# Optimization experiments

Hardware: AMD Instinct MI355X
Metric: run time of the kernel (lower is better)

## Reference

```python
import jax, jax.numpy as jnp
import numpy as np

N_NODES = 50000
N_EDGES = 800000
IN_CH = 256
OUT_CH = 128
HID = 2 * OUT_CH  # 256
LN_EPS = 1e-5


def _add_self_loops(edge_index, n):
    loop = jnp.arange(n, dtype=edge_index.dtype)
    src = jnp.concatenate([edge_index[0], loop])
    dst = jnp.concatenate([edge_index[1], loop])
    return src, dst


def _gcn_norm(src, dst, n):
    # PyG GCNConv norm: deg over source index, symmetric normalization
    ones = jnp.ones(src.shape[0], dtype=jnp.float32)
    deg = jax.ops.segment_sum(ones, src, num_segments=n)
    dinv = jnp.where(deg > 0, deg ** -0.5, 0.0)
    return dinv[src] * dinv[dst]  # [E+N]


def _gcn_conv(x, src, dst, norm, w, b, gamma=None, beta=None):
    h = x @ w                              # [N, out]
    msgs = norm[:, None] * h[src]          # gather + scale, [E+N, out]
    out = jax.ops.segment_sum(msgs, dst, num_segments=x.shape[0])
    if gamma is not None:
        out = gamma * out + beta           # FiLM modulation (per-feature)
    return out + b


def _layernorm(x):
    mu = jnp.mean(x, axis=-1, keepdims=True)
    var = jnp.var(x, axis=-1, keepdims=True)
    return (x - mu) * jax.lax.rsqrt(var + LN_EPS)


def setup_inputs() -> dict:
    key = jax.random.key(0)
    ks = jax.random.split(key, 20)

    def g(k, shape, scale=0.05):
        return jax.random.normal(k, shape, dtype=jnp.float32) * scale

    x = jax.random.normal(ks[0], (N_NODES, IN_CH), dtype=jnp.float32)
    edge_index = jax.random.randint(ks[1], (2, N_EDGES), 0, N_NODES, dtype=jnp.int64)
    return {
        "x": x,
        "edge_index": edge_index,
        "conv1_w": g(ks[2], (IN_CH, HID)),
        "conv1_b": g(ks[3], (HID,)),
        "conv2_w": g(ks[4], (HID, OUT_CH)),
        "conv2_b": g(ks[5], (OUT_CH,)),
        "sig_conv_w": g(ks[6], (IN_CH, HID)),
        "sig_conv_b": g(ks[7], (HID,)),
        "fc1_w": g(ks[8], (HID, HID)),
        "fc1_b": g(ks[9], (HID,)),
        "fc2_w": g(ks[10], (HID, HID)),
        "fc2_b": g(ks[11], (HID,)),
        "fc3_w": g(ks[12], (OUT_CH, HID)),
        "fc3_b": g(ks[13], (OUT_CH,)),
        "fc4_w": g(ks[14], (OUT_CH, HID)),
        "fc4_b": g(ks[15], (OUT_CH,)),
    }


def reference(x, edge_index, conv1_w, conv1_b, conv2_w, conv2_b,
              sig_conv_w, sig_conv_b, fc1_w, fc1_b, fc2_w, fc2_b,
              fc3_w, fc3_b, fc4_w, fc4_b):
    n = x.shape[0]
    src, dst = _add_self_loops(edge_index, n)
    norm = _gcn_norm(src, dst, n)

    # --- GraphSignature (use_gcn_sig=True) ---
    s = jax.nn.relu(_gcn_conv(x, src, dst, norm, sig_conv_w, sig_conv_b))
    s = s.sum(0)  # [HID]
    gamma1 = jnp.tanh(s @ fc1_w.T + fc1_b)  # [HID]
    beta1 = jnp.tanh(s @ fc2_w.T + fc2_b)   # [HID]
    gamma2 = jnp.tanh(s @ fc3_w.T + fc3_b)  # [OUT]
    beta2 = jnp.tanh(s @ fc4_w.T + fc4_b)   # [OUT]

    # inner_loop=True: signature outputs are detached
    gamma1, beta1, gamma2, beta2 = map(jax.lax.stop_gradient,
                                       (gamma1, beta1, gamma2, beta2))

    # --- Encoder (GAE) ---
    h = jax.nn.relu(_gcn_conv(x, src, dst, norm, conv1_w, conv1_b,
                              gamma=gamma1, beta=beta1))
    h = _layernorm(h)
    out = _gcn_conv(h, src, dst, norm, conv2_w, conv2_b,
                    gamma=gamma2, beta=beta2)
    out = _layernorm(out)
    return out
```

## Files before the change

### kernel.cpp

```cpp
#include <hip/hip_runtime.h>

typedef _Float16 f16;
typedef f16 f16x8 __attribute__((ext_vector_type(8)));
typedef float f32x4 __attribute__((ext_vector_type(4)));
typedef unsigned short u16;
typedef unsigned int u32;

#define IN_CH  256
#define HID    256
#define OUT_CH 128
#define LN_EPS 1e-5f
#define NSLOT  32
#define NR     4
#define NC     64
#define RS     12544
#define HT     512


__global__ __launch_bounds__(HT) void k_hist(const int* __restrict__ ei, int nE, int nN,
                                             int* __restrict__ hP) {
    __shared__ int h[RS];
    int r = blockIdx.x & (NR - 1), c = blockIdx.x >> 2;
    int rsz = (nN + NR - 1) / NR;
    int r0 = r * rsz;
    int sz = nN - r0; if (sz > rsz) sz = rsz;
    for (int i = threadIdx.x; i < sz; i += HT) h[i] = 0;
    __syncthreads();
    int nT = nE + nN;
    int chunk = (nT + NC - 1) / NC;
    int e0 = c * chunk, e1 = e0 + chunk; if (e1 > nT) e1 = nT;
    for (int eb = e0 + (int)threadIdx.x; eb < e1; eb += HT * 4) {
        int ss[4], dd[4];
        #pragma unroll
        for (int u = 0; u < 4; u++) {
            int e = eb + u * HT;
            ss[u] = -1; dd[u] = -1;
            if (e < e1) {
                if (e < nE) { ss[u] = ei[e]; dd[u] = ei[nE + e]; }
                else { ss[u] = e - nE; dd[u] = e - nE; }
            }
        }
        #pragma unroll
        for (int u = 0; u < 4; u++) {
            if ((unsigned)(ss[u] - r0) < (unsigned)sz) atomicAdd(&h[ss[u] - r0], 1);
            if ((unsigned)(dd[u] - r0) < (unsigned)sz) atomicAdd(&h[dd[u] - r0], 0x10000);
        }
    }
    __syncthreads();
    for (int i = threadIdx.x; i < sz; i += HT) hP[(size_t)c * nN + r0 + i] = h[i];
}


__global__ __launch_bounds__(256) void k_alloc(const int* __restrict__ hP,
                                               int* __restrict__ rowstart,
                                               int* __restrict__ chunkbase,
                                               int* __restrict__ cnt_tot,
                                               float* __restrict__ dinv,
                                               int* __restrict__ ctr, int nN,
                                               const float* __restrict__ x, f16* __restrict__ xh,
                                               int nelem, int nAllocB, int nCast,
                                               const float* __restrict__ sigw,
                                               const float* __restrict__ c1w,
                                               const float* __restrict__ c2w,
                                               f16* __restrict__ Wt1, f16* __restrict__ Wt2) {
    int bid = blockIdx.x;
    if (bid < nAllocB) {
        int i = bid * 256 + threadIdx.x;
        int lane = threadIdx.x & 63;
        int cnt = 0, dg = 0;
        if (i < nN) {
            for (int c = 0; c < NC; c++) {
                unsigned pk = (unsigned)hP[(size_t)c * nN + i];
                cnt += (int)(pk >> 16);
                dg  += (int)(pk & 0xffffu);
            }
        }
        int p = cnt;
        #pragma unroll
        for (int off = 1; off < 64; off <<= 1) {
            int v = __shfl_up(p, off, 64);
            if (lane >= off) p += v;
        }
        int tot = __shfl(p, 63, 64);
        int base = 0;
        if (lane == 0) base = atomicAdd(ctr, tot);
        base = __shfl(base, 0, 64);
        if (i < nN) {
            int nb = base + p - cnt;
            rowstart[i] = nb;
            cnt_tot[i] = cnt;
            dinv[i] = rsqrtf((float)dg);
            int run = nb;
            for (int c = 0; c < NC; c++) {
                chunkbase[(size_t)c * nN + i] = run;
                run += (int)((unsigned)hP[(size_t)c * nN + i] >> 16);
            }
        }
    } else if (bid < nAllocB + nCast) {
        int i = (bid - nAllocB) * 2048 + threadIdx.x * 8;
        if (i >= nelem) return;
        float4 a = *(const float4*)(x + i);
        float4 b = *(const float4*)(x + i + 4);
        f16x8 o = { (f16)a.x, (f16)a.y, (f16)a.z, (f16)a.w,
                    (f16)b.x, (f16)b.y, (f16)b.z, (f16)b.w };
        *(f16x8*)(xh + i) = o;
    } else {
        int i = (bid - nAllocB - nCast) * 256 + threadIdx.x;
        if (i < 16384) {
            int ct = i >> 9;
            int rem = i & 511;
            int kx = rem >> 6;
            int lane = rem & 63;
            int q = lane >> 4, l = lane & 15;
            int n = (ct & 15) * 16 + l;
            int k0 = kx * 32 + q * 8;
            const float* src = (ct < 16) ? sigw : c1w;
            f16x8 o;
            #pragma unroll
            for (int j = 0; j < 8; j++) o[j] = (f16)src[(size_t)(k0 + j) * 256 + n];
            *(f16x8*)(Wt1 + (size_t)i * 8) = o;
        } else {
            int h = i - 16384;
            int ct = h >> 9;
            int rem = h & 511;
            int kx = rem >> 6;
            int lane = rem & 63;
            int q = lane >> 4, l = lane & 15;
            int n = ct * 16 + l;
            int k0 = kx * 32 + q * 8;
            f16x8 o;
            #pragma unroll
            for (int j = 0; j < 8; j++) o[j] = (f16)c2w[(size_t)(k0 + j) * 128 + n];
            *(f16x8*)(Wt2 + (size_t)h * 8) = o;
        }
    }
}


__global__ __launch_bounds__(HT) void k_fill(const int* __restrict__ ei, int nE, int nN,
                                             const int* __restrict__ chunkbase,
                                             u16* __restrict__ src_sorted) {
    __shared__ int pos_[RS];
    int r = blockIdx.x & (NR - 1), c = blockIdx.x >> 2;
    int rsz = (nN + NR - 1) / NR;
    int r0 = r * rsz;
    int sz = nN - r0; if (sz > rsz) sz = rsz;
    for (int i = threadIdx.x; i < sz; i += HT)
        pos_[i] = chunkbase[(size_t)c * nN + r0 + i];
    __syncthreads();
    int nT = nE + nN;
    int chunk = (nT + NC - 1) / NC;
    int e0 = c * chunk, e1 = e0 + chunk; if (e1 > nT) e1 = nT;
    for (int eb = e0 + (int)threadIdx.x; eb < e1; eb += HT * 4) {
        int ss[4], dd[4];
        #pragma unroll
        for (int u = 0; u < 4; u++) {
            int e = eb + u * HT;
            ss[u] = -1; dd[u] = -1;
            if (e < e1) {
                if (e < nE) { ss[u] = ei[e]; dd[u] = ei[nE + e]; }
                else { ss[u] = e - nE; dd[u] = e - nE; }
            }
        }
        #pragma unroll
        for (int u = 0; u < 4; u++) {
            int l = dd[u] - r0;
            if ((unsigned)l < (unsigned)sz) {
                int pos = atomicAdd(&pos_[l], 1);
                src_sorted[pos] = (u16)ss[u];
            }
        }
    }
}


__global__ __launch_bounds__(256) void k_aggX(const f16* __restrict__ xh,
                                              const int* __restrict__ rowstart,
                                              const int* __restrict__ counts,
                                              const u16* __restrict__ srcs,
                                              const float* __restrict__ dinv,
                                              f16* __restrict__ AX, int nN) {
    int wv = threadIdx.x >> 6;
    int lane = threadIdx.x & 63;
    int node = blockIdx.x * 4 + wv;
    if (node >= nN) return;
    int h = lane >> 5, sub = lane & 31;
    int beg = rowstart[node];
    int cnt = counts[node];
    float acc0[8] = {}, acc1[8] = {};
    for (int base = 0; base < cnt; base += 64) {
        int el = base + lane;
        int sv = 0; float dv = 0.f;
        if (el < cnt) { sv = srcs[beg + el]; dv = dinv[sv]; }
        int rem = cnt - base; if (rem > 64) rem = 64;
        int e = 0;
        for (; e + 16 <= rem; e += 16) {
            int s_[8]; float n_[8];
            #pragma unroll
            for (int u = 0; u < 8; u++) {
                int ii = e + u * 2 + h;
                s_[u] = __shfl(sv, ii, 64);
                n_[u] = __shfl(dv, ii, 64);
            }
            f16x8 v_[8];
            #pragma unroll
            for (int u = 0; u < 8; u++)
                v_[u] = *(const f16x8*)(xh + (size_t)s_[u] * 256 + sub * 8);
            #pragma unroll
            for (int u = 0; u < 8; u++)
                #pragma unroll
                for (int j = 0; j < 8; j++) {
                    float* a = (u & 1) ? acc1 : acc0;
                    a[j] = fmaf(n_[u], (float)v_[u][j], a[j]);
                }
        }
        for (; e < rem; e += 8) {
            int i0 = e + h, i1 = e + 2 + h, i2 = e + 4 + h, i3 = e + 6 + h;
            int sa = __shfl(sv, i0, 64), sb = __shfl(sv, i1, 64);
            int sc = __shfl(sv, i2, 64), sd = __shfl(sv, i3, 64);
            float na = __shfl(dv, i0, 64), nb = __shfl(dv, i1, 64);
            float nc = __shfl(dv, i2, 64), nd = __shfl(dv, i3, 64);
            if (i0 >= rem) na = 0.f;
            if (i1 >= rem) nb = 0.f;
            if (i2 >= rem) nc = 0.f;
            if (i3 >= rem) nd = 0.f;
            f16x8 va = *(const f16x8*)(xh + (size_t)sa * 256 + sub * 8);
            f16x8 vb = *(const f16x8*)(xh + (size_t)sb * 256 + sub * 8);
            f16x8 vc = *(const f16x8*)(xh + (size_t)sc * 256 + sub * 8);
            f16x8 vd = *(const f16x8*)(xh + (size_t)sd * 256 + sub * 8);
            #pragma unroll
            for (int j = 0; j < 8; j++) {
                acc0[j] = fmaf(na, (float)va[j], acc0[j]);
                acc1[j] = fmaf(nb, (float)vb[j], acc1[j]);
                acc0[j] = fmaf(nc, (float)vc[j], acc0[j]);
                acc1[j] = fmaf(nd, (float)vd[j], acc1[j]);
            }
        }
    }
    float dn = dinv[node];
    #pragma unroll
    for (int j = 0; j < 8; j++) {
        acc0[j] += acc1[j];
        acc0[j] += __shfl_xor(acc0[j], 32, 64);
    }
    if (lane < 32) {
        f16x8 o;
        #pragma unroll
        for (int j = 0; j < 8; j++) o[j] = (f16)(acc0[j] * dn);
        *(f16x8*)(AX + (size_t)node * 256 + sub * 8) = o;
    }
}


__global__ __launch_bounds__(256) void k_gemm_sig(const f16* __restrict__ AX,
                                                  const f16* __restrict__ Wt,
                                                  const float* __restrict__ sigb,
                                                  float* __restrict__ sig_part, int M) {
    __shared__ f16 axs[32][256];
    __shared__ f16 tile[32][264];
    f16* axl = &axs[0][0];
    int t = threadIdx.x;
    int w = t >> 6, lane = t & 63, quad = lane >> 4, l16 = lane & 15;
    int m0 = blockIdx.x * 32;
    {
        int tr = t >> 5;
        int c  = t & 31;
        #pragma unroll
        for (int p = 0; p < 4; p++) {
            int row = p * 8 + tr;
            int grow = m0 + row; if (grow >= M) grow = M - 1;
            *(f16x8*)(axl + row * 256 + ((c ^ tr) << 3)) =
                *(const f16x8*)(AX + (size_t)grow * 256 + c * 8);
        }
    }
    __syncthreads();
    int cb = w * 64;
    int sw = l16 & 7;
    f32x4 acc[2][4] = {};
    for (int kx = 0; kx < 8; kx++) {
        int c0 = (kx * 4 + quad) ^ sw;
        f16x8 a[2];
        a[0] = *(const f16x8*)(axl + l16 * 256 + (c0 << 3));
        a[1] = *(const f16x8*)(axl + (16 + l16) * 256 + (c0 << 3));
        #pragma unroll
        for (int ns = 0; ns < 4; ns++) {
            int ct = w * 4 + ns;
            f16x8 b = *(const f16x8*)(Wt + ((size_t)((ct * 8 + kx) * 64 + lane) << 3));
            acc[0][ns] = __builtin_amdgcn_mfma_f32_16x16x32_f16(a[0], b, acc[0][ns], 0, 0, 0);
            acc[1][ns] = __builtin_amdgcn_mfma_f32_16x16x32_f16(a[1], b, acc[1][ns], 0, 0, 0);
        }
    }
    #pragma unroll
    for (int ms = 0; ms < 2; ms++)
        #pragma unroll
        for (int ns = 0; ns < 4; ns++)
            #pragma unroll
            for (int r = 0; r < 4; r++) {
                int mr = ms * 16 + quad * 4 + r;
                int c = cb + ns * 16 + l16;
                float v = fmaxf(acc[ms][ns][r] + sigb[c], 0.f);
                if (m0 + mr >= M) v = 0.f;
                tile[mr][c] = (f16)v;
            }
    __syncthreads();
    float s = 0.f;
    #pragma unroll 8
    for (int r = 0; r < 32; r++) s += (float)tile[r][t];
    atomicAdd(&sig_part[(blockIdx.x & (NSLOT - 1)) * 256 + t], s);
}


__global__ __launch_bounds__(256) void k_fc(const float* __restrict__ sig_part,
                                            const float* __restrict__ f1w, const float* __restrict__ f1b,
                                            const float* __restrict__ f2w, const float* __restrict__ f2b,
                                            const float* __restrict__ f3w, const float* __restrict__ f3b,
                                            const float* __restrict__ f4w, const float* __restrict__ f4b,
                                            const float* __restrict__ c1b, const float* __restrict__ c2b,
                                            float* __restrict__ g1, float* __restrict__ bc1,
                                            float* __restrict__ g2, float* __restrict__ bc2) {
    __shared__ float ss[256];
    int t = threadIdx.x;
    float s = 0.f;
    for (int k = 0; k < NSLOT; k++) s += sig_part[k * 256 + t];
    ss[t] = s;
    __syncthreads();
    int wv = t >> 6, lane = t & 63;
    float s0 = ss[lane], s1 = ss[lane + 64], s2v = ss[lane + 128], s3 = ss[lane + 192];
    #pragma unroll
    for (int rr = 0; rr < 16; rr++) {
        int row = blockIdx.x * 64 + wv * 16 + rr;
        const float* w; const float* bb; const float* ex; float* dst; int r;
        if (row < 256)      { w = f1w; bb = f1b; dst = g1;  ex = 0;   r = row; }
        else if (row < 512) { w = f2w; bb = f2b; dst = bc1; ex = c1b; r = row - 256; }
        else if (row < 640) { w = f3w; bb = f3b; dst = g2;  ex = 0;   r = row - 512; }
        else                { w = f4w; bb = f4b; dst = bc2; ex = c2b; r = row - 640; }
        const float* wr = w + (size_t)r * 256;
        float a = wr[lane] * s0;
        a = fmaf(wr[lane + 64], s1, a);
        a = fmaf(wr[lane + 128], s2v, a);
        a = fmaf(wr[lane + 192], s3, a);
        #pragma unroll
        for (int off = 1; off < 64; off <<= 1) a += __shfl_xor(a, off, 64);
        if (lane == 0) dst[r] = tanhf(a + bb[r]) + (ex ? ex[r] : 0.f);
    }
}


__global__ __launch_bounds__(256) void k_c1f(const f16* __restrict__ AX,
                                             const f16* __restrict__ Wt,
                                             const f16* __restrict__ Wt2,
                                             const float* __restrict__ g1,
                                             const float* __restrict__ bc1,
                                             const float* __restrict__ dinv,
                                             f16* __restrict__ HW, int M) {
    __shared__ f16 axs[32][256];
    __shared__ f16 ht[32][264];
    __shared__ float ps[32][5], ps2[32][5];
    __shared__ float mu_[32], rr_[32], sdinv[32];
    f16* axl = &axs[0][0];
    int t = threadIdx.x;
    int w = t >> 6, lane = t & 63, quad = lane >> 4, l16 = lane & 15;
    int m0 = blockIdx.x * 32;
    int cb = w * 64;
    {
        int tr = t >> 5;
        int c  = t & 31;
        #pragma unroll
        for (int p = 0; p < 4; p++) {
            int row = p * 8 + tr;
            int grow = m0 + row; if (grow >= M) grow = M - 1;
            *(f16x8*)(axl + row * 256 + ((c ^ tr) << 3)) =
                *(const f16x8*)(AX + (size_t)grow * 256 + c * 8);
        }
    }
    __syncthreads();
    int sw = l16 & 7;
    f32x4 acc[2][4] = {};
    for (int kx = 0; kx < 8; kx++) {
        int c0 = (kx * 4 + quad) ^ sw;
        f16x8 a[2];
        a[0] = *(const f16x8*)(axl + l16 * 256 + (c0 << 3));
        a[1] = *(const f16x8*)(axl + (16 + l16) * 256 + (c0 << 3));
        #pragma unroll
        for (int ns = 0; ns < 4; ns++) {
            int ct = w * 4 + ns;
            f16x8 b = *(const f16x8*)(Wt + ((size_t)((ct * 8 + kx) * 64 + lane) << 3));
            acc[0][ns] = __builtin_amdgcn_mfma_f32_16x16x32_f16(a[0], b, acc[0][ns], 0, 0, 0);
            acc[1][ns] = __builtin_amdgcn_mfma_f32_16x16x32_f16(a[1], b, acc[1][ns], 0, 0, 0);
        }
    }

    float rs[2][4] = {{0.f,0.f,0.f,0.f},{0.f,0.f,0.f,0.f}};
    float rs2[2][4] = {{0.f,0.f,0.f,0.f},{0.f,0.f,0.f,0.f}};
    #pragma unroll
    for (int ns = 0; ns < 4; ns++) {
        int c = cb + ns * 16 + l16;
        float gv = g1[c], bv = bc1[c];
        #pragma unroll
        for (int ms = 0; ms < 2; ms++)
            #pragma unroll
            for (int r = 0; r < 4; r++) {
                float v = fmaxf(fmaf(gv, acc[ms][ns][r], bv), 0.f);
                acc[ms][ns][r] = v;
                rs[ms][r] += v;
                rs2[ms][r] = fmaf(v, v, rs2[ms][r]);
            }
    }
    #pragma unroll
    for (int off = 1; off < 16; off <<= 1)
        #pragma unroll
        for (int ms = 0; ms < 2; ms++)
            #pragma unroll
            for (int r = 0; r < 4; r++) {
                rs[ms][r]  += __shfl_xor(rs[ms][r], off, 64);
                rs2[ms][r] += __shfl_xor(rs2[ms][r], off, 64);
            }
    if (l16 == 0) {
        #pragma unroll
        for (int ms = 0; ms < 2; ms++)
            #pragma unroll
            for (int r = 0; r < 4; r++) {
                int mr = ms * 16 + quad * 4 + r;
                ps[mr][w] = rs[ms][r];
                ps2[mr][w] = rs2[ms][r];
            }
    }
    __syncthreads();
    if (t < 32) {
        float S = ps[t][0] + ps[t][1] + ps[t][2] + ps[t][3];
        float S2 = ps2[t][0] + ps2[t][1] + ps2[t][2] + ps2[t][3];
        float mu = S * (1.f / 256.f);
        mu_[t] = mu;
        rr_[t] = rsqrtf(S2 * (1.f / 256.f) - mu * mu + LN_EPS);
        int m = m0 + t;
        sdinv[t] = (m < M) ? dinv[m] : 0.f;
    }
    __syncthreads();
    #pragma unroll
    for (int ms = 0; ms < 2; ms++)
        #pragma unroll
        for (int r = 0; r < 4; r++) {
            int mr = ms * 16 + quad * 4 + r;
            float mu = mu_[mr], rr = rr_[mr];
            #pragma unroll
            for (int ns = 0; ns < 4; ns++)
                ht[mr][cb + ns * 16 + l16] = (f16)((acc[ms][ns][r] - mu) * rr);
        }
    __syncthreads();
    int cb2 = w * 32;
    f32x4 acc2[2][2] = {};
    for (int kx = 0; kx < 8; kx++) {
        int ka = kx * 32 + quad * 8;
        f16x8 a[2];
        #pragma unroll
        for (int ms = 0; ms < 2; ms++)
            a[ms] = *(const f16x8*)(&ht[ms * 16 + l16][ka]);
        #pragma unroll
        for (int ns = 0; ns < 2; ns++) {
            int ct = w * 2 + ns;
            f16x8 b = *(const f16x8*)(Wt2 + ((size_t)((ct * 8 + kx) * 64 + lane) << 3));
            acc2[0][ns] = __builtin_amdgcn_mfma_f32_16x16x32_f16(a[0], b, acc2[0][ns], 0, 0, 0);
            acc2[1][ns] = __builtin_amdgcn_mfma_f32_16x16x32_f16(a[1], b, acc2[1][ns], 0, 0, 0);
        }
    }
    #pragma unroll
    for (int ms = 0; ms < 2; ms++)
        #pragma unroll
        for (int ns = 0; ns < 2; ns++)
            #pragma unroll
            for (int r = 0; r < 4; r++) {
                int mr = ms * 16 + quad * 4 + r;
                int m = m0 + mr;
                if (m < M) HW[(size_t)m * 128 + cb2 + ns * 16 + l16] = (f16)(acc2[ms][ns][r] * sdinv[mr]);
            }
}


__global__ __launch_bounds__(256) void k_agg2(const f16* __restrict__ HW,
                                              const int* __restrict__ rowstart,
                                              const int* __restrict__ counts,
                                              const u16* __restrict__ srcs,
                                              const float* __restrict__ dinv,
                                              const float* __restrict__ g2,
                                              const float* __restrict__ bc2,
                                              float* __restrict__ out, int nN) {
    int wv = threadIdx.x >> 6;
    int lane = threadIdx.x & 63;
    int node = blockIdx.x * 4 + wv;
    if (node >= nN) return;
    int q = lane >> 4, sub = lane & 15;
    int beg = rowstart[node];
    int cnt = counts[node];
    float acc0[8] = {}, acc1[8] = {};
    for (int base = 0; base < cnt; base += 64) {
        int el = base + lane;
        int sv = 0; float dv = 0.f;
        if (el < cnt) { sv = srcs[beg + el]; dv = 1.f; }
        int rem = cnt - base; if (rem > 64) rem = 64;
        int e = 0;
        for (; e + 16 <= rem; e += 16) {
            int s_[4]; float n_[4];
            #pragma unroll
            for (int u = 0; u < 4; u++) {
                int ii = e + u * 4 + q;
                s_[u] = __shfl(sv, ii, 64);
                n_[u] = __shfl(dv, ii, 64);
            }
            f16x8 v_[4];
            #pragma unroll
            for (int u = 0; u < 4; u++)
                v_[u] = *(const f16x8*)(HW + (size_t)s_[u] * 128 + sub * 8);
            #pragma unroll
            for (int u = 0; u < 4; u++)
                #pragma unroll
                for (int j = 0; j < 8; j++) {
                    float* a = (u & 1) ? acc1 : acc0;
                    a[j] = fmaf(n_[u], (float)v_[u][j], a[j]);
                }
        }
        for (; e < rem; e += 8) {
            int i0 = e + q, i1 = e + 4 + q;
            int sa = __shfl(sv, i0, 64), sb = __shfl(sv, i1, 64);
            float na = __shfl(dv, i0, 64), nb = __shfl(dv, i1, 64);
            if (i0 >= rem) na = 0.f;
            if (i1 >= rem) nb = 0.f;
            f16x8 va = *(const f16x8*)(HW + (size_t)sa * 128 + sub * 8);
            f16x8 vb = *(const f16x8*)(HW + (size_t)sb * 128 + sub * 8);
            #pragma unroll
            for (int j = 0; j < 8; j++) {
                acc0[j] = fmaf(na, (float)va[j], acc0[j]);
                acc1[j] = fmaf(nb, (float)vb[j], acc1[j]);
            }
        }
    }
    float dn = dinv[node];
    #pragma unroll
    for (int j = 0; j < 8; j++) {
        acc0[j] += acc1[j];
        acc0[j] += __shfl_xor(acc0[j], 16, 64);
        acc0[j] += __shfl_xor(acc0[j], 32, 64);
    }
    int ch = sub * 8;
    float vfin[8];
    float s = 0.f, s2 = 0.f;
    #pragma unroll
    for (int j = 0; j < 8; j++) {
        float v = fmaf(g2[ch + j], acc0[j] * dn, bc2[ch + j]);
        vfin[j] = v;
        s += v; s2 = fmaf(v, v, s2);
    }
    #pragma unroll
    for (int off = 1; off < 16; off <<= 1) {
        s += __shfl_xor(s, off, 64);
        s2 += __shfl_xor(s2, off, 64);
    }
    float mu = s * (1.f / 128.f);
    float rr = rsqrtf(s2 * (1.f / 128.f) - mu * mu + LN_EPS);
    if (q == 0) {
        float4 o0 = { (vfin[0] - mu) * rr, (vfin[1] - mu) * rr,
                      (vfin[2] - mu) * rr, (vfin[3] - mu) * rr };
        float4 o1 = { (vfin[4] - mu) * rr, (vfin[5] - mu) * rr,
                      (vfin[6] - mu) * rr, (vfin[7] - mu) * rr };
        float* dst = out + (size_t)node * 128 + ch;
        *(float4*)dst = o0;
        *(float4*)(dst + 4) = o1;
    }
}


extern "C" void kernel_launch(void* const* d_in, const int* in_sizes, int n_in,
                              void* d_out, int out_size, void* d_ws, size_t ws_size,
                              hipStream_t stream) {
    const float* x    = (const float*)d_in[0];
    const int*   ei   = (const int*)d_in[1];
    const float* c1w  = (const float*)d_in[2];
    const float* c1b  = (const float*)d_in[3];
    const float* c2w  = (const float*)d_in[4];
    const float* c2b  = (const float*)d_in[5];
    const float* sigw = (const float*)d_in[6];
    const float* sigb = (const float*)d_in[7];
    const float* f1w  = (const float*)d_in[8];
    const float* f1b  = (const float*)d_in[9];
    const float* f2w  = (const float*)d_in[10];
    const float* f2b  = (const float*)d_in[11];
    const float* f3w  = (const float*)d_in[12];
    const float* f3b  = (const float*)d_in[13];
    const float* f4w  = (const float*)d_in[14];
    const float* f4b  = (const float*)d_in[15];
    float* out = (float*)d_out;

    int nN = in_sizes[0] / IN_CH;
    int nE = in_sizes[1] / 2;
    int nT = nE + nN;

    char* base = (char*)d_ws;
    size_t off = 0;
    auto alloc = [&](size_t bytes) { size_t o = off; off += (bytes + 255) & ~(size_t)255; return o; };

    size_t o_spart  = alloc((size_t)NSLOT * 256 * 4);
    size_t o_ctr    = alloc(256);
    size_t zero_bytes = off;
    size_t o_hP     = alloc((size_t)NC * nN * 4);
    size_t o_cbase  = alloc((size_t)NC * nN * 4);
    size_t o_g1     = alloc(256 * 4);
    size_t o_b1     = alloc(256 * 4);
    size_t o_g2     = alloc(128 * 4);
    size_t o_b2     = alloc(128 * 4);
    size_t o_rowst  = alloc((size_t)nN * 4);
    size_t o_cntt   = alloc((size_t)nN * 4);
    size_t o_dinv   = alloc((size_t)nN * 4);
    size_t o_src    = alloc((size_t)nT * 2);
    size_t o_wt1    = alloc(512 * 256 * 2);
    size_t o_wt2    = alloc(128 * 256 * 2);
    size_t o_xh     = alloc((size_t)nN * 256 * 2);
    size_t o_AX     = alloc((size_t)nN * 256 * 2);
    size_t o_HW     = alloc((size_t)nN * 128 * 2);

    float* spart  = (float*)(base + o_spart);
    int*   ctr    = (int*)(base + o_ctr);
    int*   hP     = (int*)(base + o_hP);
    int*   cbase  = (int*)(base + o_cbase);
    float* g1     = (float*)(base + o_g1);
    float* bc1    = (float*)(base + o_b1);
    float* g2     = (float*)(base + o_g2);
    float* bc2    = (float*)(base + o_b2);
    int*   rowst  = (int*)(base + o_rowst);
    int*   cntt   = (int*)(base + o_cntt);
    float* dinv   = (float*)(base + o_dinv);
    u16*   srcs   = (u16*)(base + o_src);
    f16*   Wt1    = (f16*)(base + o_wt1);
    f16*   Wt2    = (f16*)(base + o_wt2);
    f16*   xh     = (f16*)(base + o_xh);
    f16*   AX     = (f16*)(base + o_AX);
    f16*   HW     = (f16*)(base + o_HW);

    hipMemsetAsync(base, 0, zero_bytes, stream);

    k_hist<<<NR * NC, HT, 0, stream>>>(ei, nE, nN, hP);

    int nAllocB = (nN + 255) / 256;
    int nCast = (nN * IN_CH + 2047) / 2048;
    int nPrep = (512 * 256 + 128 * 256) / 2048;
    k_alloc<<<nAllocB + nCast + nPrep, 256, 0, stream>>>(hP, rowst, cbase, cntt, dinv, ctr, nN,
                                                         x, xh, nN * IN_CH, nAllocB, nCast,
                                                         sigw, c1w, c2w, Wt1, Wt2);

    k_fill<<<NR * NC, HT, 0, stream>>>(ei, nE, nN, cbase, srcs);

    int nb4 = (nN + 3) / 4;
    int mg = (nN + 31) / 32;
    k_aggX<<<nb4, 256, 0, stream>>>(xh, rowst, cntt, srcs, dinv, AX, nN);
    k_gemm_sig<<<mg, 256, 0, stream>>>(AX, Wt1, sigb, spart, nN);
    k_fc<<<12, 256, 0, stream>>>(spart, f1w, f1b, f2w, f2b, f3w, f3b, f4w, f4b,
                                 c1b, c2b, g1, bc1, g2, bc2);
    k_c1f<<<mg, 256, 0, stream>>>(AX, Wt1 + 256 * 256, Wt2, g1, bc1, dinv, HW, nN);
    k_agg2<<<nb4, 256, 0, stream>>>(HW, rowst, cntt, srcs, dinv, g2, bc2, out, nN);
}
```

Measured before the change: 311.9 us.

## Move x cast and weight prep into histogram kernel; halve chunk count

The fp16 cast of x and the weight transpose/cast now run as extra blocks in the histogram kernel, so they overlap with the edge histogram instead of with the prefix/alloc kernel. The histogram partition changes from 4 node ranges by 64 edge chunks to 8 ranges by 32 chunks, which halves the per-chunk partial histogram that k_alloc reads and writes. The trade-off is that each edge chunk is now scanned by 8 blocks instead of 4, so total edge reads in the histogram and fill kernels go up, and shared memory per block drops.

```diff
diff --git a/kernel.cpp b/kernel.cpp
--- a/kernel.cpp
+++ b/kernel.cpp
@@ -11,93 +11,53 @@
 #define OUT_CH 128
 #define LN_EPS 1e-5f
 #define NSLOT  32
-#define NR     4
-#define NC     64
-#define RS     12544
+#define NR     8
+#define NC     32
+#define RS     6272
 #define HT     512
 
 
 __global__ __launch_bounds__(HT) void k_hist(const int* __restrict__ ei, int nE, int nN,
-                                             int* __restrict__ hP) {
-    __shared__ int h[RS];
-    int r = blockIdx.x & (NR - 1), c = blockIdx.x >> 2;
-    int rsz = (nN + NR - 1) / NR;
-    int r0 = r * rsz;
-    int sz = nN - r0; if (sz > rsz) sz = rsz;
-    for (int i = threadIdx.x; i < sz; i += HT) h[i] = 0;
-    __syncthreads();
-    int nT = nE + nN;
-    int chunk = (nT + NC - 1) / NC;
-    int e0 = c * chunk, e1 = e0 + chunk; if (e1 > nT) e1 = nT;
-    for (int eb = e0 + (int)threadIdx.x; eb < e1; eb += HT * 4) {
-        int ss[4], dd[4];
-        #pragma unroll
-        for (int u = 0; u < 4; u++) {
-            int e = eb + u * HT;
-            ss[u] = -1; dd[u] = -1;
-            if (e < e1) {
-                if (e < nE) { ss[u] = ei[e]; dd[u] = ei[nE + e]; }
-                else { ss[u] = e - nE; dd[u] = e - nE; }
-            }
-        }
-        #pragma unroll
-        for (int u = 0; u < 4; u++) {
-            if ((unsigned)(ss[u] - r0) < (unsigned)sz) atomicAdd(&h[ss[u] - r0], 1);
-            if ((unsigned)(dd[u] - r0) < (unsigned)sz) atomicAdd(&h[dd[u] - r0], 0x10000);
-        }
-    }
-    __syncthreads();
-    for (int i = threadIdx.x; i < sz; i += HT) hP[(size_t)c * nN + r0 + i] = h[i];
-}
-
-
-__global__ __launch_bounds__(256) void k_alloc(const int* __restrict__ hP,
-                                               int* __restrict__ rowstart,
-                                               int* __restrict__ chunkbase,
-                                               int* __restrict__ cnt_tot,
-                                               float* __restrict__ dinv,
-                                               int* __restrict__ ctr, int nN,
-                                               const float* __restrict__ x, f16* __restrict__ xh,
-                                               int nelem, int nAllocB, int nCast,
-                                               const float* __restrict__ sigw,
-                                               const float* __restrict__ c1w,
-                                               const float* __restrict__ c2w,
-                                               f16* __restrict__ Wt1, f16* __restrict__ Wt2) {
+                                             int* __restrict__ hP,
+                                             const float* __restrict__ x, f16* __restrict__ xh,
+                                             int nelem, int nCast,
+                                             const float* __restrict__ sigw,
+                                             const float* __restrict__ c1w,
+                                             const float* __restrict__ c2w,
+                                             f16* __restrict__ Wt1, f16* __restrict__ Wt2) {
     int bid = blockIdx.x;
-    if (bid < nAllocB) {
-        int i = bid * 256 + threadIdx.x;
-        int lane = threadIdx.x & 63;
-        int cnt = 0, dg = 0;
-        if (i < nN) {
-            for (int c = 0; c < NC; c++) {
-                unsigned pk = (unsigned)hP[(size_t)c * nN + i];
-                cnt += (int)(pk >> 16);
-                dg  += (int)(pk & 0xffffu);
-            }
-        }
-        int p = cnt;
-        #pragma unroll
-        for (int off = 1; off < 64; off <<= 1) {
-            int v = __shfl_up(p, off, 64);
-            if (lane >= off) p += v;
-        }
-        int tot = __shfl(p, 63, 64);
-        int base = 0;
-        if (lane == 0) base = atomicAdd(ctr, tot);
-        base = __shfl(base, 0, 64);
-        if (i < nN) {
-            int nb = base + p - cnt;
-            rowstart[i] = nb;
-            cnt_tot[i] = cnt;
-            dinv[i] = rsqrtf((float)dg);
-            int run = nb;
-            for (int c = 0; c < NC; c++) {
-                chunkbase[(size_t)c * nN + i] = run;
-                run += (int)((unsigned)hP[(size_t)c * nN + i] >> 16);
-            }
-        }
-    } else if (bid < nAllocB + nCast) {
-        int i = (bid - nAllocB) * 2048 + threadIdx.x * 8;
+    if (bid < NR * NC) {
+        __shared__ int h[RS];
+        int r = bid & (NR - 1), c = bid >> 3;
+        int rsz = (nN + NR - 1) / NR;
+        int r0 = r * rsz;
+        int sz = nN - r0; if (sz > rsz) sz = rsz;
+        for (int i = threadIdx.x; i < sz; i += HT) h[i] = 0;
+        __syncthreads();
+        int nT = nE + nN;
+        int chunk = (nT + NC - 1) / NC;
+        int e0 = c * chunk, e1 = e0 + chunk; if (e1 > nT) e1 = nT;
+        for (int eb = e0 + (int)threadIdx.x; eb < e1; eb += HT * 4) {
+            int ss[4], dd[4];
+            #pragma unroll
+            for (int u = 0; u < 4; u++) {
+                int e = eb + u * HT;
+                ss[u] = -1; dd[u] = -1;
+                if (e < e1) {
+                    if (e < nE) { ss[u] = ei[e]; dd[u] = ei[nE + e]; }
+                    else { ss[u] = e - nE; dd[u] = e - nE; }
+                }
+            }
+            #pragma unroll
+            for (int u = 0; u < 4; u++) {
+                if ((unsigned)(ss[u] - r0) < (unsigned)sz) atomicAdd(&h[ss[u] - r0], 1);
+                if ((unsigned)(dd[u] - r0) < (unsigned)sz) atomicAdd(&h[dd[u] - r0], 0x10000);
+            }
+        }
+        __syncthreads();
+        for (int i = threadIdx.x; i < sz; i += HT) hP[(size_t)c * nN + r0 + i] = h[i];
+    } else if (bid < NR * NC + nCast) {
+        int i = (bid - NR * NC) * 4096 + threadIdx.x * 8;
         if (i >= nelem) return;
         float4 a = *(const float4*)(x + i);
         float4 b = *(const float4*)(x + i + 4);
@@ -105,7 +65,7 @@
                     (f16)b.x, (f16)b.y, (f16)b.z, (f16)b.w };
         *(f16x8*)(xh + i) = o;
     } else {
-        int i = (bid - nAllocB - nCast) * 256 + threadIdx.x;
+        int i = (bid - NR * NC - nCast) * HT + threadIdx.x;
         if (i < 16384) {
             int ct = i >> 9;
             int rem = i & 511;
@@ -119,10 +79,10 @@
             #pragma unroll
             for (int j = 0; j < 8; j++) o[j] = (f16)src[(size_t)(k0 + j) * 256 + n];
             *(f16x8*)(Wt1 + (size_t)i * 8) = o;
-        } else {
-            int h = i - 16384;
-            int ct = h >> 9;
-            int rem = h & 511;
+        } else if (i < 20480) {
+            int h2 = i - 16384;
+            int ct = h2 >> 9;
+            int rem = h2 & 511;
             int kx = rem >> 6;
             int lane = rem & 63;
             int q = lane >> 4, l = lane & 15;
@@ -131,7 +91,47 @@
             f16x8 o;
             #pragma unroll
             for (int j = 0; j < 8; j++) o[j] = (f16)c2w[(size_t)(k0 + j) * 128 + n];
-            *(f16x8*)(Wt2 + (size_t)h * 8) = o;
+            *(f16x8*)(Wt2 + (size_t)h2 * 8) = o;
+        }
+    }
+}
+
+
+__global__ __launch_bounds__(256) void k_alloc(const int* __restrict__ hP,
+                                               int* __restrict__ rowstart,
+                                               int* __restrict__ chunkbase,
+                                               int* __restrict__ cnt_tot,
+                                               float* __restrict__ dinv,
+                                               int* __restrict__ ctr, int nN) {
+    int i = blockIdx.x * 256 + threadIdx.x;
+    int lane = threadIdx.x & 63;
+    int cnt = 0, dg = 0;
+    if (i < nN) {
+        for (int c = 0; c < NC; c++) {
+            unsigned pk = (unsigned)hP[(size_t)c * nN + i];
+            cnt += (int)(pk >> 16);
+            dg  += (int)(pk & 0xffffu);
+        }
+    }
+    int p = cnt;
+    #pragma unroll
+    for (int off = 1; off < 64; off <<= 1) {
+        int v = __shfl_up(p, off, 64);
+        if (lane >= off) p += v;
+    }
+    int tot = __shfl(p, 63, 64);
+    int base = 0;
+    if (lane == 0) base = atomicAdd(ctr, tot);
+    base = __shfl(base, 0, 64);
+    if (i < nN) {
+        int nb = base + p - cnt;
+        rowstart[i] = nb;
+        cnt_tot[i] = cnt;
+        dinv[i] = rsqrtf((float)dg);
+        int run = nb;
+        for (int c = 0; c < NC; c++) {
+            chunkbase[(size_t)c * nN + i] = run;
+            run += (int)((unsigned)hP[(size_t)c * nN + i] >> 16);
         }
     }
 }
@@ -141,7 +141,7 @@
                                              const int* __restrict__ chunkbase,
                                              u16* __restrict__ src_sorted) {
     __shared__ int pos_[RS];
-    int r = blockIdx.x & (NR - 1), c = blockIdx.x >> 2;
+    int r = blockIdx.x & (NR - 1), c = blockIdx.x >> 3;
     int rsz = (nN + NR - 1) / NR;
     int r0 = r * rsz;
     int sz = nN - r0; if (sz > rsz) sz = rsz;
@@ -636,14 +636,13 @@
 
     hipMemsetAsync(base, 0, zero_bytes, stream);
 
-    k_hist<<<NR * NC, HT, 0, stream>>>(ei, nE, nN, hP);
-
-    int nAllocB = (nN + 255) / 256;
-    int nCast = (nN * IN_CH + 2047) / 2048;
-    int nPrep = (512 * 256 + 128 * 256) / 2048;
-    k_alloc<<<nAllocB + nCast + nPrep, 256, 0, stream>>>(hP, rowst, cbase, cntt, dinv, ctr, nN,
-                                                         x, xh, nN * IN_CH, nAllocB, nCast,
-                                                         sigw, c1w, c2w, Wt1, Wt2);
+    int nCast = (nN * IN_CH + 4095) / 4096;
+    int nPrep = (20480 + HT - 1) / HT;
+    k_hist<<<NR * NC + nCast + nPrep, HT, 0, stream>>>(ei, nE, nN, hP,
+                                                       x, xh, nN * IN_CH, nCast,
+                                                       sigw, c1w, c2w, Wt1, Wt2);
+
+    k_alloc<<<(nN + 255) / 256, 256, 0, stream>>>(hP, rowst, cbase, cntt, dinv, ctr, nN);
 
     k_fill<<<NR * NC, HT, 0, stream>>>(ei, nE, nN, cbase, srcs);
 
```

Result: no change. 310.3 us (-0.5%).
